# Optimization experiments

Measured on AMD Instinct MI355X. Metric: run time of the kernel, lower is better.

Reference implementation:

```python
import jax, jax.numpy as jnp
import numpy as np

N_NODES = 50000
N_EDGES = 800000
NUM_FEATURES = 128
HIDDEN = 128
NUM_GRAPHS = 500


def setup_inputs() -> dict:
    key = jax.random.key(0)
    ks = jax.random.split(key, 8)
    def lin_w(k, fan_in, fan_out):
        bound = 1.0 / np.sqrt(fan_in)
        return jax.random.uniform(k, (fan_in, fan_out), jnp.float32, -bound, bound)
    x = jax.random.normal(ks[0], (N_NODES, NUM_FEATURES), jnp.float32)
    W0 = lin_w(ks[1], NUM_FEATURES, HIDDEN)
    W1 = lin_w(ks[2], HIDDEN, HIDDEN)
    W2 = lin_w(ks[3], HIDDEN, HIDDEN)
    Wout = lin_w(ks[4], HIDDEN, 1)
    b0 = jnp.zeros((HIDDEN,), jnp.float32)
    b1 = jnp.zeros((HIDDEN,), jnp.float32)
    b2 = jnp.zeros((HIDDEN,), jnp.float32)
    bout = jnp.zeros((1,), jnp.float32)
    edge_index = jax.random.randint(ks[5], (2, N_EDGES), 0, N_NODES, jnp.int64)
    batch = jnp.sort(jax.random.randint(ks[6], (N_NODES,), 0, NUM_GRAPHS, jnp.int64))
    return {"x": x, "W0": W0, "b0": b0, "W1": W1, "b1": b1, "W2": W2,
            "b2": b2, "Wout": Wout, "bout": bout,
            "edge_index": edge_index, "batch": batch}


def _gcn_conv(x, W, b, row, col, norm, n_nodes):
    # GCNConv: out = D^{-1/2} (A + I) D^{-1/2} X W + b
    xw = x @ W                                  # [N, H] dense GEMM
    msg = xw[row] * norm[:, None]               # gather + scale  [E+N, H]
    out = jax.ops.segment_sum(msg, col, num_segments=n_nodes)  # scatter-add
    return out + b


def _gcn_norm(edge_index, n_nodes):
    # add self-loops, then symmetric degree normalization
    loops = jnp.arange(n_nodes, dtype=edge_index.dtype)
    row = jnp.concatenate([edge_index[0], loops])  # source (j)
    col = jnp.concatenate([edge_index[1], loops])  # target (i)
    deg = jax.ops.segment_sum(jnp.ones_like(col, dtype=jnp.float32), col,
                              num_segments=n_nodes)
    dinv = jnp.where(deg > 0, jax.lax.rsqrt(jnp.maximum(deg, 1.0)), 0.0)
    norm = dinv[row] * dinv[col]
    return row, col, norm


def reference(x, W0, b0, W1, b1, W2, b2, Wout, bout, edge_index, batch):
    n_nodes = x.shape[0]
    row, col, norm = _gcn_norm(edge_index, n_nodes)
    h = x
    for (W, b) in ((W0, b0), (W1, b1), (W2, b2)):
        h = _gcn_conv(h, W, b, row, col, norm, n_nodes)
        h = jax.nn.elu(h)
        # F.dropout(training=False) -> identity in eval mode
    # global_mean_pool over graph ids
    sums = jax.ops.segment_sum(h, batch, num_segments=NUM_GRAPHS)
    cnts = jax.ops.segment_sum(jnp.ones((n_nodes,), h.dtype), batch,
                               num_segments=NUM_GRAPHS)
    pooled = sums / jnp.maximum(cnts, 1.0)[:, None]   # [G, H]
    return pooled @ Wout + bout                       # [G, 1]
```

## Files before the change

kernel.cpp:

```cpp
#include <hip/hip_runtime.h>
#include <math.h>

#define NN 50000
#define NE 800000
#define HD 128
#define NG 500
#define CAP 48

__global__ void k_fill(const int* __restrict__ erow, const int* __restrict__ ecol,
                       int* __restrict__ deg, unsigned short* __restrict__ rec) {
    int e = blockIdx.x * blockDim.x + threadIdx.x;
    if (e < NE) {
        int r = erow[e];
        int c = ecol[e];
        int p = atomicAdd(&deg[c], 1);
        p = p < CAP - 1 ? p : CAP - 1;
        rec[c * CAP + p] = (unsigned short)r;
    }
}

__global__ void k_prep(const int* __restrict__ deg, float* __restrict__ dinv,
                       const int* __restrict__ batch, int* __restrict__ gptr) {
    int i = blockIdx.x * blockDim.x + threadIdx.x;
    if (i < NN) dinv[i] = rsqrtf((float)(deg[i] + 1));
    if (i <= NG) {
        int lo = 0, hi = NN;
        while (lo < hi) {
            int mid = (lo + hi) >> 1;
            if (batch[mid] < i) lo = mid + 1; else hi = mid;
        }
        gptr[i] = lo;
    }
}

__global__ __launch_bounds__(256) void k_gemm(const float* __restrict__ Hin,
                                              const float* __restrict__ W,
                                              const float* __restrict__ dinv,
                                              float* __restrict__ XW) {
    __shared__ float Hs[64][36];
    __shared__ float Ws[32][132];

    const int tid = threadIdx.x;
    const int base = blockIdx.x * 64;
    const int tr = tid >> 4;
    const int tc = tid & 15;
    const int c0 = tc * 8;

    float acc[4][8];
#pragma unroll
    for (int i = 0; i < 4; ++i)
#pragma unroll
        for (int j = 0; j < 8; ++j) acc[i][j] = 0.f;

    for (int kc = 0; kc < 4; ++kc) {
        __syncthreads();
#pragma unroll
        for (int i = 0; i < 2; ++i) {
            int idx = i * 256 + tid;
            int r = idx >> 3;
            int c4 = idx & 7;
            int row = base + r;
            float4 v = make_float4(0.f, 0.f, 0.f, 0.f);
            if (row < NN) v = *(const float4*)(Hin + (size_t)row * HD + kc * 32 + c4 * 4);
            *(float4*)&Hs[r][c4 * 4] = v;
        }
#pragma unroll
        for (int i = 0; i < 4; ++i) {
            int idx = i * 256 + tid;
            int kr = idx >> 5;
            int c4 = idx & 31;
            float4 v = *(const float4*)(W + (size_t)(kc * 32 + kr) * HD + c4 * 4);
            *(float4*)&Ws[kr][c4 * 4] = v;
        }
        __syncthreads();
#pragma unroll
        for (int k4 = 0; k4 < 8; ++k4) {
            float ha[4][4];
#pragma unroll
            for (int i = 0; i < 4; ++i) {
                float4 hv = *(const float4*)&Hs[tr + 16 * i][k4 * 4];
                ha[i][0] = hv.x; ha[i][1] = hv.y; ha[i][2] = hv.z; ha[i][3] = hv.w;
            }
#pragma unroll
            for (int q = 0; q < 4; ++q) {
                float4 w0 = *(const float4*)&Ws[k4 * 4 + q][c0];
                float4 w1 = *(const float4*)&Ws[k4 * 4 + q][c0 + 4];
                float wa[8] = {w0.x, w0.y, w0.z, w0.w, w1.x, w1.y, w1.z, w1.w};
#pragma unroll
                for (int i = 0; i < 4; ++i) {
                    float hv = ha[i][q];
#pragma unroll
                    for (int j = 0; j < 8; ++j) acc[i][j] += hv * wa[j];
                }
            }
        }
    }

#pragma unroll
    for (int i = 0; i < 4; ++i) {
        int row = base + tr + 16 * i;
        if (row >= NN) continue;
        float d = dinv[row];
        float4 x0 = make_float4(acc[i][0] * d, acc[i][1] * d, acc[i][2] * d, acc[i][3] * d);
        float4 x1 = make_float4(acc[i][4] * d, acc[i][5] * d, acc[i][6] * d, acc[i][7] * d);
        *(float4*)(XW + (size_t)row * HD + c0)     = x0;
        *(float4*)(XW + (size_t)row * HD + c0 + 4) = x1;
    }
}

__device__ __forceinline__ float2 gather_acc(const float* __restrict__ XW,
                                             const unsigned short* __restrict__ rec,
                                             int bb, int deg, int lane) {
    float2 acc = make_float2(0.f, 0.f);
    for (int j = 0; j < deg; j += 8) {
        int src[8];
        float sc[8];
#pragma unroll
        for (int k = 0; k < 8; ++k) {
            int jj = j + k;
            bool ok = jj < deg;
            src[k] = rec[bb + (ok ? jj : 0)];
            sc[k] = ok ? 1.f : 0.f;
        }
        float2 v[8];
#pragma unroll
        for (int k = 0; k < 8; ++k)
            v[k] = ((const float2*)(XW + (size_t)src[k] * HD))[lane];
#pragma unroll
        for (int k = 0; k < 8; ++k) {
            acc.x += v[k].x * sc[k];
            acc.y += v[k].y * sc[k];
        }
    }
    return acc;
}

__global__ __launch_bounds__(256) void k_gather(const float* __restrict__ XW,
                                                float* __restrict__ B,
                                                const unsigned short* __restrict__ rec,
                                                const int* __restrict__ deg,
                                                const float* __restrict__ dinv,
                                                const float* __restrict__ bias) {
    int node = blockIdx.x * 4 + (threadIdx.x >> 6);
    int lane = threadIdx.x & 63;
    if (node >= NN) return;
    float2 acc = gather_acc(XW, rec, node * CAP, deg[node], lane);
    float d = dinv[node];
    float2 xi = ((const float2*)(XW + (size_t)node * HD))[lane];
    float2 bb = ((const float2*)bias)[lane];
    float2 h;
    h.x = d * (acc.x + xi.x) + bb.x;
    h.y = d * (acc.y + xi.y) + bb.y;
    h.x = h.x > 0.f ? h.x : expm1f(h.x);
    h.y = h.y > 0.f ? h.y : expm1f(h.y);
    ((float2*)(B + (size_t)node * HD))[lane] = h;
}

__global__ __launch_bounds__(256) void k_gather_pool(const float* __restrict__ XW,
                                                     const unsigned short* __restrict__ rec,
                                                     const int* __restrict__ deg,
                                                     const float* __restrict__ dinv,
                                                     const float* __restrict__ bias,
                                                     const float* __restrict__ Wout,
                                                     float* __restrict__ nodedot) {
    int node = blockIdx.x * 4 + (threadIdx.x >> 6);
    int lane = threadIdx.x & 63;
    if (node >= NN) return;
    float2 acc = gather_acc(XW, rec, node * CAP, deg[node], lane);
    float d = dinv[node];
    float2 xi = ((const float2*)(XW + (size_t)node * HD))[lane];
    float2 bb = ((const float2*)bias)[lane];
    float2 h;
    h.x = d * (acc.x + xi.x) + bb.x;
    h.y = d * (acc.y + xi.y) + bb.y;
    h.x = h.x > 0.f ? h.x : expm1f(h.x);
    h.y = h.y > 0.f ? h.y : expm1f(h.y);
    float2 w = ((const float2*)Wout)[lane];
    float v = h.x * w.x + h.y * w.y;
#pragma unroll
    for (int off = 32; off > 0; off >>= 1) v += __shfl_down(v, off);
    if (lane == 0) nodedot[node] = v;
}

__global__ __launch_bounds__(64) void k_pool2(const float* __restrict__ nodedot,
                                              const int* __restrict__ gptr,
                                              const float* __restrict__ bout,
                                              float* __restrict__ out) {
    int g = blockIdx.x;
    int lane = threadIdx.x;
    int s = gptr[g];
    int e = gptr[g + 1];
    float acc = 0.f;
    for (int i = s + lane; i < e; i += 64) acc += nodedot[i];
#pragma unroll
    for (int off = 32; off > 0; off >>= 1) acc += __shfl_down(acc, off);
    if (lane == 0) {
        int c = e - s;
        out[g] = acc / (float)(c > 0 ? c : 1) + bout[0];
    }
}

extern "C" void kernel_launch(void* const* d_in, const int* in_sizes, int n_in,
                              void* d_out, int out_size, void* d_ws, size_t ws_size,
                              hipStream_t stream) {
    const float* x    = (const float*)d_in[0];
    const float* W0   = (const float*)d_in[1];
    const float* b0   = (const float*)d_in[2];
    const float* W1   = (const float*)d_in[3];
    const float* b1   = (const float*)d_in[4];
    const float* W2   = (const float*)d_in[5];
    const float* b2   = (const float*)d_in[6];
    const float* Wout = (const float*)d_in[7];
    const float* bout = (const float*)d_in[8];
    const int*   erow = (const int*)d_in[9];
    const int*   ecol = erow + NE;
    const int*   batch = (const int*)d_in[10];
    float* out = (float*)d_out;

    float* A       = (float*)d_ws;
    float* B       = A + (size_t)NN * HD;
    float* dinv    = B + (size_t)NN * HD;
    int*   deg     = (int*)(dinv + NN);
    float* nodedot = (float*)(deg + NN);
    int*   gptr    = (int*)(nodedot + NN);
    unsigned short* rec = (unsigned short*)(gptr + NG + 1);

    hipMemsetAsync(deg, 0, NN * sizeof(int), stream);
    k_fill<<<(NE + 255) / 256, 256, 0, stream>>>(erow, ecol, deg, rec);
    k_prep<<<(NN + 255) / 256, 256, 0, stream>>>(deg, dinv, batch, gptr);

    const float* Hin = x;
    const float* Wl[3] = {W0, W1, W2};
    const float* bl[3] = {b0, b1, b2};
    for (int l = 0; l < 2; ++l) {
        k_gemm<<<(NN + 63) / 64, 256, 0, stream>>>(Hin, Wl[l], dinv, A);
        k_gather<<<(NN + 3) / 4, 256, 0, stream>>>(A, B, rec, deg, dinv, bl[l]);
        Hin = B;
    }
    k_gemm<<<(NN + 63) / 64, 256, 0, stream>>>(Hin, Wl[2], dinv, A);
    k_gather_pool<<<(NN + 3) / 4, 256, 0, stream>>>(A, rec, deg, dinv, bl[2],
                                                    Wout, nodedot);
    k_pool2<<<NG, 64, 0, stream>>>(nodedot, gptr, bout, out);
}
```

Measured before the change: 332.2 us.

## Overlap first-layer GEMM with edge CSR fill in one fused front kernel

```diff
diff --git a/kernel.cpp b/kernel.cpp
--- a/kernel.cpp
+++ b/kernel.cpp
@@ -6,36 +6,146 @@
 #define HD 128
 #define NG 500
 #define CAP 48
-
-__global__ void k_fill(const int* __restrict__ erow, const int* __restrict__ ecol,
-                       int* __restrict__ deg, unsigned short* __restrict__ rec) {
-    int e = blockIdx.x * blockDim.x + threadIdx.x;
-    if (e < NE) {
-        int r = erow[e];
-        int c = ecol[e];
-        int p = atomicAdd(&deg[c], 1);
-        p = p < CAP - 1 ? p : CAP - 1;
-        rec[c * CAP + p] = (unsigned short)r;
-    }
-}
-
-__global__ void k_prep(const int* __restrict__ deg, float* __restrict__ dinv,
-                       const int* __restrict__ batch, int* __restrict__ gptr) {
-    int i = blockIdx.x * blockDim.x + threadIdx.x;
-    if (i < NN) dinv[i] = rsqrtf((float)(deg[i] + 1));
-    if (i <= NG) {
+#define GEMM_BLKS 782
+#define FILL_BLKS 384
+#define FRONT_GRID (GEMM_BLKS + FILL_BLKS)
+
+__global__ __launch_bounds__(256) void k_front(const float* __restrict__ x,
+                                               const float* __restrict__ W,
+                                               const int* __restrict__ erow,
+                                               const int* __restrict__ ecol,
+                                               int* __restrict__ deg,
+                                               unsigned short* __restrict__ rec,
+                                               float* __restrict__ XW) {
+    __shared__ float Hs[64][36];
+    __shared__ float Ws[32][132];
+
+    const int bid = blockIdx.x;
+    const int tid = threadIdx.x;
+
+    if (bid >= GEMM_BLKS) {
+        for (int e = (bid - GEMM_BLKS) * 256 + tid; e < NE; e += FILL_BLKS * 256) {
+            int r = erow[e];
+            int c = ecol[e];
+            int p = atomicAdd(&deg[c], 1);
+            p = p < CAP - 1 ? p : CAP - 1;
+            rec[c * CAP + p] = (unsigned short)r;
+        }
+        return;
+    }
+
+    const int base = bid * 64;
+    const int tr = tid >> 4;
+    const int tc = tid & 15;
+    const int c0 = tc * 8;
+
+    float acc[4][8];
+#pragma unroll
+    for (int i = 0; i < 4; ++i)
+#pragma unroll
+        for (int j = 0; j < 8; ++j) acc[i][j] = 0.f;
+
+    for (int kc = 0; kc < 4; ++kc) {
+        __syncthreads();
+#pragma unroll
+        for (int i = 0; i < 2; ++i) {
+            int idx = i * 256 + tid;
+            int r = idx >> 3;
+            int c4 = idx & 7;
+            int row = base + r;
+            float4 v = make_float4(0.f, 0.f, 0.f, 0.f);
+            if (row < NN) v = *(const float4*)(x + (size_t)row * HD + kc * 32 + c4 * 4);
+            *(float4*)&Hs[r][c4 * 4] = v;
+        }
+#pragma unroll
+        for (int i = 0; i < 4; ++i) {
+            int idx = i * 256 + tid;
+            int kr = idx >> 5;
+            int c4 = idx & 31;
+            float4 v = *(const float4*)(W + (size_t)(kc * 32 + kr) * HD + c4 * 4);
+            *(float4*)&Ws[kr][c4 * 4] = v;
+        }
+        __syncthreads();
+#pragma unroll
+        for (int k4 = 0; k4 < 8; ++k4) {
+            float ha[4][4];
+#pragma unroll
+            for (int i = 0; i < 4; ++i) {
+                float4 hv = *(const float4*)&Hs[tr + 16 * i][k4 * 4];
+                ha[i][0] = hv.x; ha[i][1] = hv.y; ha[i][2] = hv.z; ha[i][3] = hv.w;
+            }
+#pragma unroll
+            for (int q = 0; q < 4; ++q) {
+                float4 w0 = *(const float4*)&Ws[k4 * 4 + q][c0];
+                float4 w1 = *(const float4*)&Ws[k4 * 4 + q][c0 + 4];
+                float wa[8] = {w0.x, w0.y, w0.z, w0.w, w1.x, w1.y, w1.z, w1.w};
+#pragma unroll
+                for (int i = 0; i < 4; ++i) {
+                    float hv = ha[i][q];
+#pragma unroll
+                    for (int j = 0; j < 8; ++j) acc[i][j] += hv * wa[j];
+                }
+            }
+        }
+    }
+
+#pragma unroll
+    for (int i = 0; i < 4; ++i) {
+        int row = base + tr + 16 * i;
+        if (row >= NN) continue;
+        float4 x0 = make_float4(acc[i][0], acc[i][1], acc[i][2], acc[i][3]);
+        float4 x1 = make_float4(acc[i][4], acc[i][5], acc[i][6], acc[i][7]);
+        *(float4*)(XW + (size_t)row * HD + c0)     = x0;
+        *(float4*)(XW + (size_t)row * HD + c0 + 4) = x1;
+    }
+}
+
+__global__ __launch_bounds__(256) void k_prep_scale(const int* __restrict__ deg,
+                                                    float* __restrict__ dinv,
+                                                    const int* __restrict__ batch,
+                                                    int* __restrict__ gptr,
+                                                    float* __restrict__ A) {
+    __shared__ float sdinv[64];
+    const int bid = blockIdx.x;
+    const int tid = threadIdx.x;
+
+    if (tid < 64) {
+        int row = bid * 64 + tid;
+        float d = 0.f;
+        if (row < NN) {
+            d = rsqrtf((float)(deg[row] + 1));
+            dinv[row] = d;
+        }
+        sdinv[tid] = d;
+    }
+    int flat = bid * 256 + tid;
+    if (flat <= NG) {
         int lo = 0, hi = NN;
         while (lo < hi) {
             int mid = (lo + hi) >> 1;
-            if (batch[mid] < i) lo = mid + 1; else hi = mid;
-        }
-        gptr[i] = lo;
+            if (batch[mid] < flat) lo = mid + 1; else hi = mid;
+        }
+        gptr[flat] = lo;
+    }
+    __syncthreads();
+
+#pragma unroll
+    for (int i = 0; i < 8; ++i) {
+        int idx = i * 256 + tid;
+        int r = idx >> 5;
+        int c4 = idx & 31;
+        int row = bid * 64 + r;
+        if (row < NN) {
+            float d = sdinv[r];
+            float4 v = *(const float4*)(A + (size_t)row * HD + c4 * 4);
+            v.x *= d; v.y *= d; v.z *= d; v.w *= d;
+            *(float4*)(A + (size_t)row * HD + c4 * 4) = v;
+        }
     }
 }
 
 __global__ __launch_bounds__(256) void k_gemm(const float* __restrict__ Hin,
                                               const float* __restrict__ W,
-                                              const float* __restrict__ dinv,
                                               float* __restrict__ XW) {
     __shared__ float Hs[64][36];
     __shared__ float Ws[32][132];
@@ -100,9 +210,8 @@
     for (int i = 0; i < 4; ++i) {
         int row = base + tr + 16 * i;
         if (row >= NN) continue;
-        float d = dinv[row];
-        float4 x0 = make_float4(acc[i][0] * d, acc[i][1] * d, acc[i][2] * d, acc[i][3] * d);
-        float4 x1 = make_float4(acc[i][4] * d, acc[i][5] * d, acc[i][6] * d, acc[i][7] * d);
+        float4 x0 = make_float4(acc[i][0], acc[i][1], acc[i][2], acc[i][3]);
+        float4 x1 = make_float4(acc[i][4], acc[i][5], acc[i][6], acc[i][7]);
         *(float4*)(XW + (size_t)row * HD + c0)     = x0;
         *(float4*)(XW + (size_t)row * HD + c0 + 4) = x1;
     }
@@ -153,6 +262,8 @@
     h.y = d * (acc.y + xi.y) + bb.y;
     h.x = h.x > 0.f ? h.x : expm1f(h.x);
     h.y = h.y > 0.f ? h.y : expm1f(h.y);
+    h.x *= d;
+    h.y *= d;
     ((float2*)(B + (size_t)node * HD))[lane] = h;
 }
 
@@ -226,19 +337,14 @@
     unsigned short* rec = (unsigned short*)(gptr + NG + 1);
 
     hipMemsetAsync(deg, 0, NN * sizeof(int), stream);
-    k_fill<<<(NE + 255) / 256, 256, 0, stream>>>(erow, ecol, deg, rec);
-    k_prep<<<(NN + 255) / 256, 256, 0, stream>>>(deg, dinv, batch, gptr);
-
-    const float* Hin = x;
-    const float* Wl[3] = {W0, W1, W2};
-    const float* bl[3] = {b0, b1, b2};
-    for (int l = 0; l < 2; ++l) {
-        k_gemm<<<(NN + 63) / 64, 256, 0, stream>>>(Hin, Wl[l], dinv, A);
-        k_gather<<<(NN + 3) / 4, 256, 0, stream>>>(A, B, rec, deg, dinv, bl[l]);
-        Hin = B;
-    }
-    k_gemm<<<(NN + 63) / 64, 256, 0, stream>>>(Hin, Wl[2], dinv, A);
-    k_gather_pool<<<(NN + 3) / 4, 256, 0, stream>>>(A, rec, deg, dinv, bl[2],
+    k_front<<<FRONT_GRID, 256, 0, stream>>>(x, W0, erow, ecol, deg, rec, A);
+    k_prep_scale<<<GEMM_BLKS, 256, 0, stream>>>(deg, dinv, batch, gptr, A);
+
+    k_gather<<<(NN + 3) / 4, 256, 0, stream>>>(A, B, rec, deg, dinv, b0);
+    k_gemm<<<(NN + 63) / 64, 256, 0, stream>>>(B, W1, A);
+    k_gather<<<(NN + 3) / 4, 256, 0, stream>>>(A, B, rec, deg, dinv, b1);
+    k_gemm<<<(NN + 63) / 64, 256, 0, stream>>>(B, W2, A);
+    k_gather_pool<<<(NN + 3) / 4, 256, 0, stream>>>(A, rec, deg, dinv, b2,
                                                     Wout, nodedot);
     k_pool2<<<NG, 64, 0, stream>>>(nodedot, gptr, bout, out);
 }
```

Measured after the change: 298.6 us (median of 2 runs). 10.1% less time.
